# Kernel tuning notes

Hardware: AMD Instinct MI355X
Metric: run time of the kernel (lower is better)

## Reference

```python
import jax, jax.numpy as jnp
import numpy as np

N_GRAPHS = 32   # number of graphs (equal-size contiguous segments in `batch`)
SEG_LEN = 512   # nodes per graph
NUM_HEADS = 16
LN_EPS = 1e-5


def setup_inputs() -> dict:
    key = jax.random.key(0)
    ks = jax.random.split(key, 4)
    N = N_GRAPHS * SEG_LEN
    D = 1024
    x = jax.random.normal(ks[0], (N, D), dtype=jnp.float32)
    # contiguous equal-size graph segments (what per-graph batching produces)
    batch = jnp.repeat(jnp.arange(N_GRAPHS, dtype=jnp.int64), SEG_LEN)
    s = 1.0 / np.sqrt(D)
    w_in = jax.random.normal(ks[1], (3 * D, D), dtype=jnp.float32) * s
    b_in = jnp.zeros((3 * D,), dtype=jnp.float32)
    w_out = jax.random.normal(ks[2], (D, D), dtype=jnp.float32) * s
    b_out = jnp.zeros((D,), dtype=jnp.float32)
    gamma = jnp.ones((D,), dtype=jnp.float32)
    beta = jnp.zeros((D,), dtype=jnp.float32)
    return {"x": x, "batch": batch, "w_in": w_in, "b_in": b_in,
            "w_out": w_out, "b_out": b_out, "gamma": gamma, "beta": beta}


def _mha_blockdiag(x, w_in, b_in, w_out, b_out):
    # Packed per-graph self-attention: identical math to looping MHA over each
    # graph's node subset, but done in one dense batched attention.
    N, D = x.shape
    G, S, H = N_GRAPHS, SEG_LEN, NUM_HEADS
    dh = D // H
    qkv = x @ w_in.T + b_in                       # (N, 3D)
    qkv = qkv.reshape(G, S, 3, H, dh)
    q, k, v = qkv[:, :, 0], qkv[:, :, 1], qkv[:, :, 2]  # (G, S, H, dh)
    scale = 1.0 / jnp.sqrt(jnp.asarray(dh, x.dtype))
    scores = jnp.einsum('gqhd,gkhd->ghqk', q, k) * scale  # (G, H, S, S)
    probs = jax.nn.softmax(scores, axis=-1)
    ctx = jnp.einsum('ghqk,gkhd->gqhd', probs, v).reshape(N, D)
    return ctx @ w_out.T + b_out


def reference(x, batch, w_in, b_in, w_out, b_out, gamma, beta):
    attn_out = _mha_blockdiag(x, w_in, b_in, w_out, b_out)
    # dropout is identity in eval mode; residual + LayerNorm
    h = x + attn_out
    mu = jnp.mean(h, axis=-1, keepdims=True)
    var = jnp.var(h, axis=-1, keepdims=True)
    return (h - mu) * jax.lax.rsqrt(var + LN_EPS) * gamma + beta
```

## Files before the change

### kernel.cpp

```cpp
#include <hip/hip_runtime.h>
#include <hip/hip_bf16.h>
#include <math.h>

#define N_TOK  16384
#define DMODEL 1024
#define GRAPHS 32
#define SEGLEN 512
#define HEADS  16
#define DH     64
#define D3     3072
#define QK_LD  2048
#define KDIM   1024
#define NT_K   16

typedef __bf16 bf16;
typedef __attribute__((ext_vector_type(4))) __bf16 bf16x4;
typedef __attribute__((ext_vector_type(8))) __bf16 bf16x8;
typedef __attribute__((ext_vector_type(4))) float f32x4;

__global__ __launch_bounds__(256) void cvt_f32_bf16(const float* __restrict__ in,
                                                    bf16* __restrict__ out, int n4) {
    int i = blockIdx.x * blockDim.x + threadIdx.x;
    if (i < n4) {
        float4 v = ((const float4*)in)[i];
        bf16x4 o;
        o[0] = (bf16)v.x; o[1] = (bf16)v.y; o[2] = (bf16)v.z; o[3] = (bf16)v.w;
        ((bf16x4*)out)[i] = o;
    }
}

template<int EPI, int VSPLIT, int CVT_A>
__global__ __launch_bounds__(256, 3) void gemm128(
    const void* __restrict__ Ap, const bf16* __restrict__ B,
    const float* __restrict__ bias, const float* __restrict__ resid,
    void* __restrict__ C, bf16* __restrict__ vT, int N, int nbn, int ldc)
{
    __shared__ bf16x8 smA[1024];
    __shared__ bf16x8 smB[1024];
    const int tid  = threadIdx.x;
    const int lane = tid & 63, w = tid >> 6;
    const int wr = w >> 1, wc = w & 1;
    const int l15 = lane & 15, l4 = lane >> 4;
    const int r7 = l15 & 7;

    const int nwg = (int)gridDim.x;
    const int bid = (int)blockIdx.x;
    const int sw  = (bid & 7) * (nwg >> 3) + (bid >> 3);
    const int bm0 = (sw / nbn) * 128, bn0 = (sw % nbn) * 128;

    const int srow = tid >> 3, skb = tid & 7;

    uint4 pa0[4], pa1[4], pb[4];
    auto PF_LOAD = [&](int t) {
        const int k0 = t * 64;
        #pragma unroll
        for (int q = 0; q < 4; q++) {
            int row = q * 32 + srow;
            if (CVT_A) {
                const float* af = (const float*)Ap + (size_t)(bm0 + row) * KDIM + k0 + skb * 8;
                pa0[q] = *(const uint4*)af;
                pa1[q] = *(const uint4*)(af + 4);
            } else {
                pa0[q] = *(const uint4*)((const bf16*)Ap + (size_t)(bm0 + row) * KDIM + k0 + skb * 8);
            }
            pb[q] = *(const uint4*)(B + (size_t)(bn0 + row) * KDIM + k0 + skb * 8);
        }
    };
    auto LDS_WRITE = [&]() {
        #pragma unroll
        for (int q = 0; q < 4; q++) {
            int row = q * 32 + srow;
            bf16x8 av;
            if (CVT_A) {
                float4 lo = __builtin_bit_cast(float4, pa0[q]);
                float4 hi = __builtin_bit_cast(float4, pa1[q]);
                av[0] = (bf16)lo.x; av[1] = (bf16)lo.y; av[2] = (bf16)lo.z; av[3] = (bf16)lo.w;
                av[4] = (bf16)hi.x; av[5] = (bf16)hi.y; av[6] = (bf16)hi.z; av[7] = (bf16)hi.w;
            } else {
                av = __builtin_bit_cast(bf16x8, pa0[q]);
            }
            smA[row * 8 + (skb ^ (row & 7))] = av;
            smB[row * 8 + (skb ^ (row & 7))] = __builtin_bit_cast(bf16x8, pb[q]);
        }
    };

    f32x4 acc[4][4] = {};

    PF_LOAD(0);
    LDS_WRITE();
    __syncthreads();

    #pragma unroll 1
    for (int t = 0; t < NT_K; ++t) {
        if (t + 1 < NT_K) PF_LOAD(t + 1);
        #pragma unroll
        for (int kp = 0; kp < 2; kp++) {
            const int slot = kp * 4 + l4;
            bf16x8 af[4], bfr[4];
            #pragma unroll
            for (int m = 0; m < 4; m++)
                af[m] = smA[(wr * 64 + m * 16 + l15) * 8 + (slot ^ r7)];
            #pragma unroll
            for (int n = 0; n < 4; n++)
                bfr[n] = smB[(wc * 64 + n * 16 + l15) * 8 + (slot ^ r7)];
            #pragma unroll
            for (int m = 0; m < 4; m++)
                #pragma unroll
                for (int n = 0; n < 4; n++)
                    acc[m][n] = __builtin_amdgcn_mfma_f32_16x16x32_bf16(af[m], bfr[n], acc[m][n], 0, 0, 0);
        }
        __syncthreads();
        if (t + 1 < NT_K) {
            LDS_WRITE();
            __syncthreads();
        }
    }

    #pragma unroll
    for (int m = 0; m < 4; m++) {
        #pragma unroll
        for (int n = 0; n < 4; n++) {
            const int col  = bn0 + wc * 64 + n * 16 + l15;
            const int row0 = bm0 + wr * 64 + m * 16 + l4 * 4;
            const float bv = bias[col];
            if (EPI == 1) {
                #pragma unroll
                for (int i = 0; i < 4; i++) {
                    float v = acc[m][n][i] + bv + resid[(size_t)(row0 + i) * N + col];
                    ((bf16*)C)[(size_t)(row0 + i) * ldc + col] = (bf16)v;
                }
            } else if (VSPLIT && bn0 >= 2048) {
                const int cc = col - 2048;
                bf16x4 pk;
                #pragma unroll
                for (int i = 0; i < 4; i++) pk[i] = (bf16)(acc[m][n][i] + bv);
                *(bf16x4*)(vT + ((size_t)((row0 >> 9) * HEADS + (cc >> 6)) * DH + (cc & 63)) * SEGLEN
                               + (row0 & (SEGLEN - 1))) = pk;
            } else {
                const float sc = (VSPLIT && bn0 < 1024) ? 0.125f : 1.0f;
                #pragma unroll
                for (int i = 0; i < 4; i++)
                    ((bf16*)C)[(size_t)(row0 + i) * ldc + col] = (bf16)((acc[m][n][i] + bv) * sc);
            }
        }
    }
}

__global__ __launch_bounds__(256) void attn_kernel(
    const bf16* __restrict__ qkA, const bf16* __restrict__ vT, bf16* __restrict__ ctx)
{
    const int qt = blockIdx.x, h = blockIdx.y, g = blockIdx.z;
    __shared__ bf16x8 smQP[128 * 8];
    __shared__ bf16x8 smK[64 * 8];
    __shared__ bf16x8 smV[64 * 8];
    const int tid = threadIdx.x, lane = tid & 63, w = tid >> 6;
    const int l15 = lane & 15, l4 = lane >> 4;
    const int r7 = l15 & 7;
    const int grow0 = g * SEGLEN, qbase = qt * 128;
    const size_t vbase = (size_t)(g * HEADS + h) * DH * SEGLEN;

    #pragma unroll
    for (int q = 0; q < 4; q++) {
        int c = tid + 256 * q, r = c >> 3, cb = c & 7;
        uint4 v = *(const uint4*)(qkA + (size_t)(grow0 + qbase + r) * QK_LD + h * 64 + cb * 8);
        smQP[r * 8 + (cb ^ (r & 7))] = __builtin_bit_cast(bf16x8, v);
    }
    __syncthreads();

    bf16x8 qf[2][2];
    #pragma unroll
    for (int m = 0; m < 2; m++)
        #pragma unroll
        for (int kp = 0; kp < 2; kp++) {
            int row = w * 32 + m * 16 + l15;
            qf[m][kp] = smQP[row * 8 + ((kp * 4 + l4) ^ (row & 7))];
        }

    f32x4 acc[2][4] = {};
    float mrow[2][4], lrow[2][4];
    #pragma unroll
    for (int m = 0; m < 2; m++)
        #pragma unroll
        for (int i = 0; i < 4; i++) { mrow[m][i] = -INFINITY; lrow[m][i] = 0.f; }

    uint4 kr[2][2], vr[2][2];
    auto LOADT = [&](int t, int dst) {
        #pragma unroll
        for (int q = 0; q < 2; q++) {
            int c = tid + 256 * q, r = c >> 3, cb = c & 7;
            kr[dst][q] = *(const uint4*)(qkA + (size_t)(grow0 + t * 64 + r) * QK_LD + 1024 + h * 64 + cb * 8);
            vr[dst][q] = *(const uint4*)(vT + vbase + (size_t)r * SEGLEN + t * 64 + cb * 8);
        }
    };
    LOADT(0, 0);

    #pragma unroll
    for (int t = 0; t < 8; t++) {
        const int cur = t & 1;
        #pragma unroll
        for (int q = 0; q < 2; q++) {
            int c = tid + 256 * q, r = c >> 3, cb = c & 7;
            smK[r * 8 + (cb ^ (r & 7))] = __builtin_bit_cast(bf16x8, kr[cur][q]);
            smV[r * 8 + (cb ^ (r & 7))] = __builtin_bit_cast(bf16x8, vr[cur][q]);
        }
        if (t < 7) LOADT(t + 1, cur ^ 1);
        __syncthreads();

        f32x4 s[2][4] = {};
        #pragma unroll
        for (int kp = 0; kp < 2; kp++) {
            #pragma unroll
            for (int n = 0; n < 4; n++) {
                bf16x8 kf = smK[(n * 16 + l15) * 8 + ((kp * 4 + l4) ^ r7)];
                #pragma unroll
                for (int m = 0; m < 2; m++)
                    s[m][n] = __builtin_amdgcn_mfma_f32_16x16x32_bf16(qf[m][kp], kf, s[m][n], 0, 0, 0);
            }
        }
        float mx[2][4];
        int need = 0;
        #pragma unroll
        for (int m = 0; m < 2; m++)
            #pragma unroll
            for (int i = 0; i < 4; i++) {
                float m0 = fmaxf(fmaxf(s[m][0][i], s[m][1][i]), fmaxf(s[m][2][i], s[m][3][i]));
                #pragma unroll
                for (int d = 1; d < 16; d <<= 1) m0 = fmaxf(m0, __shfl_xor(m0, d));
                mx[m][i] = m0;
                need |= (m0 > mrow[m][i] + 8.0f) ? 1 : 0;
            }
        if (__any(need)) {
            #pragma unroll
            for (int m = 0; m < 2; m++)
                #pragma unroll
                for (int i = 0; i < 4; i++) {
                    float mn = fmaxf(mrow[m][i], mx[m][i]);
                    float alpha = __expf(mrow[m][i] - mn);
                    mrow[m][i] = mn;
                    lrow[m][i] *= alpha;
                    #pragma unroll
                    for (int n = 0; n < 4; n++) acc[m][n][i] *= alpha;
                }
        }
        float rsum[2][4] = {};
        #pragma unroll
        for (int m = 0; m < 2; m++)
            #pragma unroll
            for (int n = 0; n < 4; n++)
                #pragma unroll
                for (int i = 0; i < 4; i++) {
                    float p = __expf(s[m][n][i] - mrow[m][i]);
                    rsum[m][i] += p;
                    int prow = w * 32 + m * 16 + l4 * 4 + i;
                    ((bf16*)smQP)[prow * 64 + ((n * 16 + l15) ^ ((prow & 7) << 3))] = (bf16)p;
                }
        #pragma unroll
        for (int m = 0; m < 2; m++)
            #pragma unroll
            for (int i = 0; i < 4; i++) {
                #pragma unroll
                for (int d = 1; d < 16; d <<= 1) rsum[m][i] += __shfl_xor(rsum[m][i], d);
                lrow[m][i] += rsum[m][i];
            }
        #pragma unroll
        for (int kp = 0; kp < 2; kp++) {
            bf16x8 pf[2];
            #pragma unroll
            for (int m = 0; m < 2; m++)
                pf[m] = smQP[(w * 32 + m * 16 + l15) * 8 + ((kp * 4 + l4) ^ r7)];
            #pragma unroll
            for (int n = 0; n < 4; n++) {
                bf16x8 vf = smV[(n * 16 + l15) * 8 + ((kp * 4 + l4) ^ r7)];
                #pragma unroll
                for (int m = 0; m < 2; m++)
                    acc[m][n] = __builtin_amdgcn_mfma_f32_16x16x32_bf16(pf[m], vf, acc[m][n], 0, 0, 0);
            }
        }
        __syncthreads();
    }

    #pragma unroll
    for (int m = 0; m < 2; m++)
        #pragma unroll
        for (int i = 0; i < 4; i++) {
            float inv = 1.f / lrow[m][i];
            int row = grow0 + qbase + w * 32 + m * 16 + l4 * 4 + i;
            #pragma unroll
            for (int n = 0; n < 4; n++) {
                int col = h * 64 + n * 16 + l15;
                ctx[(size_t)row * DMODEL + col] = (bf16)(acc[m][n][i] * inv);
            }
        }
}

__global__ __launch_bounds__(256) void ln_kernel(
    const bf16* __restrict__ h, const float* __restrict__ gamma,
    const float* __restrict__ beta, float* __restrict__ out)
{
    const int row = blockIdx.x;
    bf16x4 hv = ((const bf16x4*)(h + (size_t)row * DMODEL))[threadIdx.x];
    float v0 = (float)hv[0], v1 = (float)hv[1], v2 = (float)hv[2], v3 = (float)hv[3];
    float s  = v0 + v1 + v2 + v3;
    float ss = v0 * v0 + v1 * v1 + v2 * v2 + v3 * v3;
    #pragma unroll
    for (int d = 1; d < 64; d <<= 1) { s += __shfl_xor(s, d); ss += __shfl_xor(ss, d); }
    __shared__ float red[8];
    int wv = threadIdx.x >> 6, lane = threadIdx.x & 63;
    if (lane == 0) { red[wv] = s; red[4 + wv] = ss; }
    __syncthreads();
    s  = red[0] + red[1] + red[2] + red[3];
    ss = red[4] + red[5] + red[6] + red[7];
    float mu  = s * (1.f / 1024.f);
    float var = ss * (1.f / 1024.f) - mu * mu;
    float rs  = rsqrtf(var + 1e-5f);
    float4 gv = ((const float4*)gamma)[threadIdx.x];
    float4 bv = ((const float4*)beta)[threadIdx.x];
    float4 o;
    o.x = (v0 - mu) * rs * gv.x + bv.x;
    o.y = (v1 - mu) * rs * gv.y + bv.y;
    o.z = (v2 - mu) * rs * gv.z + bv.z;
    o.w = (v3 - mu) * rs * gv.w + bv.w;
    ((float4*)(out + (size_t)row * DMODEL))[threadIdx.x] = o;
}

extern "C" void kernel_launch(void* const* d_in, const int* in_sizes, int n_in,
                              void* d_out, int out_size, void* d_ws, size_t ws_size,
                              hipStream_t stream) {
    const float* x     = (const float*)d_in[0];
    const float* w_in  = (const float*)d_in[2];
    const float* b_in  = (const float*)d_in[3];
    const float* w_out = (const float*)d_in[4];
    const float* b_out = (const float*)d_in[5];
    const float* gamma = (const float*)d_in[6];
    const float* beta  = (const float*)d_in[7];
    float* out = (float*)d_out;

    char* ws = (char*)d_ws;
    bf16*  ctxb = (bf16*)ws;
    bf16*  wb   = (bf16*)(ws + 33554432);
    bf16*  wob  = (bf16*)(ws + 39845888);
    bf16*  qkA  = (bf16*)(ws + 41943040);
    bf16*  vT   = (bf16*)(ws + 109051904);
    bf16*  hbuf = qkA;

    cvt_f32_bf16<<<3072, 256, 0, stream>>>(w_in,  wb,  D3 * DMODEL / 4);
    cvt_f32_bf16<<<1024, 256, 0, stream>>>(w_out, wob, DMODEL * DMODEL / 4);

    gemm128<0, 1, 1><<<3072, 256, 0, stream>>>(x, wb, b_in, nullptr, qkA, vT,
                                               D3, 24, QK_LD);
    attn_kernel<<<dim3(4, 16, 32), 256, 0, stream>>>(qkA, vT, ctxb);

    gemm128<1, 0, 0><<<1024, 256, 0, stream>>>(ctxb, wob, b_out, x, hbuf, nullptr,
                                               DMODEL, 8, DMODEL);
    ln_kernel<<<N_TOK, 256, 0, stream>>>(hbuf, gamma, beta, out);
}
```

Measured before the change: 332.5 us.

## Pre-convert x to bf16 in fused cast kernel; load attention K/V/Q directly from global

All three fp32-to-bf16 conversions (x, w_in, w_out) now run in one merged cast kernel, so the QKV GEMM reads bf16 A directly instead of converting fp32 inside its load loop. The attention kernel no longer stages Q, K and V through shared memory with double-buffered prefetch and block barriers. Each wave now reads MFMA fragments straight from global/L2, and only P stays in LDS. This cuts LDS traffic and syncs, but it adds a full x round trip in bf16 and replaces coalesced tile loads with strided per-lane fragment loads that depend on the cache.

```diff
diff --git a/kernel.cpp b/kernel.cpp
--- a/kernel.cpp
+++ b/kernel.cpp
@@ -18,20 +18,29 @@
 typedef __attribute__((ext_vector_type(8))) __bf16 bf16x8;
 typedef __attribute__((ext_vector_type(4))) float f32x4;
 
-__global__ __launch_bounds__(256) void cvt_f32_bf16(const float* __restrict__ in,
-                                                    bf16* __restrict__ out, int n4) {
+#define N4_X  (N_TOK * DMODEL / 4)
+#define N4_WI (D3 * DMODEL / 4)
+#define N4_WO (DMODEL * DMODEL / 4)
+__global__ __launch_bounds__(256) void cvt_all(const float* __restrict__ x,
+                                               const float* __restrict__ w_in,
+                                               const float* __restrict__ w_out,
+                                               bf16* __restrict__ xb,
+                                               bf16* __restrict__ wb,
+                                               bf16* __restrict__ wob) {
     int i = blockIdx.x * blockDim.x + threadIdx.x;
-    if (i < n4) {
-        float4 v = ((const float4*)in)[i];
-        bf16x4 o;
-        o[0] = (bf16)v.x; o[1] = (bf16)v.y; o[2] = (bf16)v.z; o[3] = (bf16)v.w;
-        ((bf16x4*)out)[i] = o;
-    }
-}
-
-template<int EPI, int VSPLIT, int CVT_A>
+    const float* src; bf16* dst; int j;
+    if (i < N4_X)                { src = x;     dst = xb;  j = i; }
+    else if (i < N4_X + N4_WI)   { src = w_in;  dst = wb;  j = i - N4_X; }
+    else                         { src = w_out; dst = wob; j = i - N4_X - N4_WI; }
+    float4 v = ((const float4*)src)[j];
+    bf16x4 o;
+    o[0] = (bf16)v.x; o[1] = (bf16)v.y; o[2] = (bf16)v.z; o[3] = (bf16)v.w;
+    ((bf16x4*)dst)[j] = o;
+}
+
+template<int EPI, int VSPLIT>
 __global__ __launch_bounds__(256, 3) void gemm128(
-    const void* __restrict__ Ap, const bf16* __restrict__ B,
+    const bf16* __restrict__ A, const bf16* __restrict__ B,
     const float* __restrict__ bias, const float* __restrict__ resid,
     void* __restrict__ C, bf16* __restrict__ vT, int N, int nbn, int ldc)
 {
@@ -50,19 +59,13 @@
 
     const int srow = tid >> 3, skb = tid & 7;
 
-    uint4 pa0[4], pa1[4], pb[4];
+    uint4 pa[4], pb[4];
     auto PF_LOAD = [&](int t) {
         const int k0 = t * 64;
         #pragma unroll
         for (int q = 0; q < 4; q++) {
             int row = q * 32 + srow;
-            if (CVT_A) {
-                const float* af = (const float*)Ap + (size_t)(bm0 + row) * KDIM + k0 + skb * 8;
-                pa0[q] = *(const uint4*)af;
-                pa1[q] = *(const uint4*)(af + 4);
-            } else {
-                pa0[q] = *(const uint4*)((const bf16*)Ap + (size_t)(bm0 + row) * KDIM + k0 + skb * 8);
-            }
+            pa[q] = *(const uint4*)(A + (size_t)(bm0 + row) * KDIM + k0 + skb * 8);
             pb[q] = *(const uint4*)(B + (size_t)(bn0 + row) * KDIM + k0 + skb * 8);
         }
     };
@@ -70,16 +73,7 @@
         #pragma unroll
         for (int q = 0; q < 4; q++) {
             int row = q * 32 + srow;
-            bf16x8 av;
-            if (CVT_A) {
-                float4 lo = __builtin_bit_cast(float4, pa0[q]);
-                float4 hi = __builtin_bit_cast(float4, pa1[q]);
-                av[0] = (bf16)lo.x; av[1] = (bf16)lo.y; av[2] = (bf16)lo.z; av[3] = (bf16)lo.w;
-                av[4] = (bf16)hi.x; av[5] = (bf16)hi.y; av[6] = (bf16)hi.z; av[7] = (bf16)hi.w;
-            } else {
-                av = __builtin_bit_cast(bf16x8, pa0[q]);
-            }
-            smA[row * 8 + (skb ^ (row & 7))] = av;
+            smA[row * 8 + (skb ^ (row & 7))] = __builtin_bit_cast(bf16x8, pa[q]);
             smB[row * 8 + (skb ^ (row & 7))] = __builtin_bit_cast(bf16x8, pb[q]);
         }
     };
@@ -150,31 +144,21 @@
     const bf16* __restrict__ qkA, const bf16* __restrict__ vT, bf16* __restrict__ ctx)
 {
     const int qt = blockIdx.x, h = blockIdx.y, g = blockIdx.z;
-    __shared__ bf16x8 smQP[128 * 8];
-    __shared__ bf16x8 smK[64 * 8];
-    __shared__ bf16x8 smV[64 * 8];
+    __shared__ bf16 smP[128 * 64];
     const int tid = threadIdx.x, lane = tid & 63, w = tid >> 6;
     const int l15 = lane & 15, l4 = lane >> 4;
     const int r7 = l15 & 7;
     const int grow0 = g * SEGLEN, qbase = qt * 128;
-    const size_t vbase = (size_t)(g * HEADS + h) * DH * SEGLEN;
-
-    #pragma unroll
-    for (int q = 0; q < 4; q++) {
-        int c = tid + 256 * q, r = c >> 3, cb = c & 7;
-        uint4 v = *(const uint4*)(qkA + (size_t)(grow0 + qbase + r) * QK_LD + h * 64 + cb * 8);
-        smQP[r * 8 + (cb ^ (r & 7))] = __builtin_bit_cast(bf16x8, v);
-    }
-    __syncthreads();
+    const bf16* kbase = qkA + (size_t)grow0 * QK_LD + 1024 + h * 64 + (size_t)l4 * 8;
+    const bf16* vbase = vT + (size_t)(g * HEADS + h) * DH * SEGLEN + (size_t)l4 * 8;
 
     bf16x8 qf[2][2];
     #pragma unroll
     for (int m = 0; m < 2; m++)
         #pragma unroll
-        for (int kp = 0; kp < 2; kp++) {
-            int row = w * 32 + m * 16 + l15;
-            qf[m][kp] = smQP[row * 8 + ((kp * 4 + l4) ^ (row & 7))];
-        }
+        for (int kp = 0; kp < 2; kp++)
+            qf[m][kp] = *(const bf16x8*)(qkA + (size_t)(grow0 + qbase + w * 32 + m * 16 + l15) * QK_LD
+                                          + h * 64 + (kp * 4 + l4) * 8);
 
     f32x4 acc[2][4] = {};
     float mrow[2][4], lrow[2][4];
@@ -183,35 +167,14 @@
         #pragma unroll
         for (int i = 0; i < 4; i++) { mrow[m][i] = -INFINITY; lrow[m][i] = 0.f; }
 
-    uint4 kr[2][2], vr[2][2];
-    auto LOADT = [&](int t, int dst) {
-        #pragma unroll
-        for (int q = 0; q < 2; q++) {
-            int c = tid + 256 * q, r = c >> 3, cb = c & 7;
-            kr[dst][q] = *(const uint4*)(qkA + (size_t)(grow0 + t * 64 + r) * QK_LD + 1024 + h * 64 + cb * 8);
-            vr[dst][q] = *(const uint4*)(vT + vbase + (size_t)r * SEGLEN + t * 64 + cb * 8);
-        }
-    };
-    LOADT(0, 0);
-
-    #pragma unroll
+    #pragma unroll 2
     for (int t = 0; t < 8; t++) {
-        const int cur = t & 1;
-        #pragma unroll
-        for (int q = 0; q < 2; q++) {
-            int c = tid + 256 * q, r = c >> 3, cb = c & 7;
-            smK[r * 8 + (cb ^ (r & 7))] = __builtin_bit_cast(bf16x8, kr[cur][q]);
-            smV[r * 8 + (cb ^ (r & 7))] = __builtin_bit_cast(bf16x8, vr[cur][q]);
-        }
-        if (t < 7) LOADT(t + 1, cur ^ 1);
-        __syncthreads();
-
         f32x4 s[2][4] = {};
         #pragma unroll
         for (int kp = 0; kp < 2; kp++) {
             #pragma unroll
             for (int n = 0; n < 4; n++) {
-                bf16x8 kf = smK[(n * 16 + l15) * 8 + ((kp * 4 + l4) ^ r7)];
+                bf16x8 kf = *(const bf16x8*)(kbase + (size_t)(t * 64 + n * 16 + l15) * QK_LD + kp * 32);
                 #pragma unroll
                 for (int m = 0; m < 2; m++)
                     s[m][n] = __builtin_amdgcn_mfma_f32_16x16x32_bf16(qf[m][kp], kf, s[m][n], 0, 0, 0);
@@ -252,7 +215,7 @@
                     float p = __expf(s[m][n][i] - mrow[m][i]);
                     rsum[m][i] += p;
                     int prow = w * 32 + m * 16 + l4 * 4 + i;
-                    ((bf16*)smQP)[prow * 64 + ((n * 16 + l15) ^ ((prow & 7) << 3))] = (bf16)p;
+                    smP[prow * 64 + ((n * 16 + l15) ^ ((prow & 7) << 3))] = (bf16)p;
                 }
         #pragma unroll
         for (int m = 0; m < 2; m++)
@@ -267,16 +230,15 @@
             bf16x8 pf[2];
             #pragma unroll
             for (int m = 0; m < 2; m++)
-                pf[m] = smQP[(w * 32 + m * 16 + l15) * 8 + ((kp * 4 + l4) ^ r7)];
+                pf[m] = ((const bf16x8*)smP)[(w * 32 + m * 16 + l15) * 8 + ((kp * 4 + l4) ^ r7)];
             #pragma unroll
             for (int n = 0; n < 4; n++) {
-                bf16x8 vf = smV[(n * 16 + l15) * 8 + ((kp * 4 + l4) ^ r7)];
+                bf16x8 vf = *(const bf16x8*)(vbase + (size_t)(n * 16 + l15) * SEGLEN + t * 64 + kp * 32);
                 #pragma unroll
                 for (int m = 0; m < 2; m++)
                     acc[m][n] = __builtin_amdgcn_mfma_f32_16x16x32_bf16(pf[m], vf, acc[m][n], 0, 0, 0);
             }
         }
-        __syncthreads();
     }
 
     #pragma unroll
@@ -336,21 +298,21 @@
     float* out = (float*)d_out;
 
     char* ws = (char*)d_ws;
-    bf16*  ctxb = (bf16*)ws;
+    bf16*  xb   = (bf16*)ws;
     bf16*  wb   = (bf16*)(ws + 33554432);
     bf16*  wob  = (bf16*)(ws + 39845888);
     bf16*  qkA  = (bf16*)(ws + 41943040);
     bf16*  vT   = (bf16*)(ws + 109051904);
+    bf16*  ctxb = xb;
     bf16*  hbuf = qkA;
 
-    cvt_f32_bf16<<<3072, 256, 0, stream>>>(w_in,  wb,  D3 * DMODEL / 4);
-    cvt_f32_bf16<<<1024, 256, 0, stream>>>(w_out, wob, DMODEL * DMODEL / 4);
-
-    gemm128<0, 1, 1><<<3072, 256, 0, stream>>>(x, wb, b_in, nullptr, qkA, vT,
-                                               D3, 24, QK_LD);
+    cvt_all<<<(N4_X + N4_WI + N4_WO) / 256, 256, 0, stream>>>(x, w_in, w_out, xb, wb, wob);
+
+    gemm128<0, 1><<<3072, 256, 0, stream>>>(xb, wb, b_in, nullptr, qkA, vT,
+                                            D3, 24, QK_LD);
     attn_kernel<<<dim3(4, 16, 32), 256, 0, stream>>>(qkA, vT, ctxb);
 
-    gemm128<1, 0, 0><<<1024, 256, 0, stream>>>(ctxb, wob, b_out, x, hbuf, nullptr,
-                                               DMODEL, 8, DMODEL);
+    gemm128<1, 0><<<1024, 256, 0, stream>>>(ctxb, wob, b_out, x, hbuf, nullptr,
+                                            DMODEL, 8, DMODEL);
     ln_kernel<<<N_TOK, 256, 0, stream>>>(hbuf, gamma, beta, out);
 }
```

New measurement: 339.4 us. 2.1% more time.
